# Kernel tuning notes

Hardware: AMD Instinct MI355X
Metric: run time of the kernel (lower is better)

Reference implementation:

```python
import jax, jax.numpy as jnp
import numpy as np

# Dims: B docs, L tokens, D hidden, H heads, NE padded entities (min_height),
# M mentions per entity, P entity pairs per doc, BLK bilinear block, NL labels.
B, L, D, H, NE, M, P = 4, 1024, 768, 12, 42, 4, 512
BLK, NL = 64, 97
OFFSET = 1  # self.offset = 1 (CLS token shift)


def setup_inputs() -> dict:
    key = jax.random.key(0)
    ks = jax.random.split(key, 10)
    sequence_output = jax.random.normal(ks[0], (B, L, D), jnp.float32)
    att = jax.random.uniform(ks[1], (B, H, L, L), jnp.float32)
    attention = att / att.sum(-1, keepdims=True)  # row-stochastic like softmax attn
    mention_pos = jax.random.randint(ks[2], (B, NE, M), 0, 1000, dtype=jnp.int32)
    hts = jax.random.randint(ks[3], (B, P, 2), 0, NE, dtype=jnp.int32)
    W_head = jax.random.normal(ks[4], (2 * D, D), jnp.float32) * 0.02
    b_head = jnp.zeros((D,), jnp.float32)
    W_tail = jax.random.normal(ks[5], (2 * D, D), jnp.float32) * 0.02
    b_tail = jnp.zeros((D,), jnp.float32)
    W_bi = jax.random.normal(ks[6], (D * BLK, NL), jnp.float32) * 0.02
    b_bi = jnp.zeros((NL,), jnp.float32)
    return dict(sequence_output=sequence_output, attention=attention,
                mention_pos=mention_pos, hts=hts,
                W_head=W_head, b_head=b_head, W_tail=W_tail, b_tail=b_tail,
                W_bi=W_bi, b_bi=b_bi)


def reference(sequence_output, attention, mention_pos, hts,
              W_head, b_head, W_tail, b_tail, W_bi, b_bi):
    pos = mention_pos + OFFSET                               # [B,NE,M]
    # --- get_hrt: entity embeds = logsumexp over mention start tokens ---
    e_emb = jax.vmap(lambda s, p: s[p])(sequence_output, pos)    # [B,NE,M,D]
    entity_embs = jax.nn.logsumexp(e_emb, axis=2)                # [B,NE,D]
    # entity attention = mean over mentions of attn rows           [B,NE,H,L]
    e_att = jax.vmap(lambda a, p: a[:, p])(attention, pos)       # [B,H,NE,M,L]
    entity_atts = e_att.mean(3).transpose(0, 2, 1, 3)            # [B,NE,H,L]
    # --- get_channel_map: ht_att = (h_att * t_att).mean(heads), normalized ---
    ht_att = jnp.einsum('bihl,bjhl->bijl', entity_atts, entity_atts) / H  # [B,NE,NE,L]
    ht_att = ht_att / (ht_att.sum(-1, keepdims=True) + 1e-5)
    rs_map = jnp.einsum('bijl,bld->bijd', ht_att, sequence_output)        # [B,NE,NE,D]
    # --- gather head/tail entity embeds and pooled context per pair ---
    h_idx, t_idx = hts[..., 0], hts[..., 1]                      # [B,P]
    hs = jnp.take_along_axis(entity_embs, h_idx[..., None], axis=1)  # [B,P,D]
    ts = jnp.take_along_axis(entity_embs, t_idx[..., None], axis=1)  # [B,P,D]
    rs = jax.vmap(lambda m, h, t: m[h, t])(rs_map, h_idx, t_idx)     # [B,P,D]
    # --- extractors + grouped bilinear classifier ---
    zs = jnp.tanh(jnp.concatenate([hs, rs], -1) @ W_head + b_head)   # [B,P,D]
    zo = jnp.tanh(jnp.concatenate([ts, rs], -1) @ W_tail + b_tail)   # [B,P,D]
    b1 = zs.reshape(B, P, D // BLK, BLK)
    b2 = zo.reshape(B, P, D // BLK, BLK)
    bl = (b1[..., :, None] * b2[..., None, :]).reshape(B, P, D * BLK)
    logits = bl @ W_bi + b_bi                                        # [B,P,NL]
    return logits
```

## Files before the change

### kernel.cpp

```cpp
#include <hip/hip_runtime.h>

constexpr int Bc = 4, Lc = 1024, Dc = 768, Hc = 12, NEc = 42, Mc = 4, Pc = 512, NLc = 97;
constexpr int BE   = Bc * NEc;
constexpr int BEp  = 176;
constexpr int ROWS = Bc * Pc;
constexpr int N2   = 2 * Dc;

typedef __attribute__((ext_vector_type(8))) short short8;
typedef _Float16 half8 __attribute__((ext_vector_type(8)));
typedef __attribute__((ext_vector_type(4))) float f32x4;

__device__ __forceinline__ f32x4 mfma_bf(short8 a, short8 b, f32x4 c) {
    return __builtin_amdgcn_mfma_f32_16x16x32_bf16(a, b, c, 0, 0, 0);
}
__device__ __forceinline__ f32x4 mfma_h(half8 a, half8 b, f32x4 c) {
    return __builtin_amdgcn_mfma_f32_16x16x32_f16(a, b, c, 0, 0, 0);
}
__device__ __forceinline__ unsigned short f2bf(float x) {
    unsigned int u = __float_as_uint(x);
    return (unsigned short)((u + 0x7fffu + ((u >> 16) & 1u)) >> 16);
}
__device__ __forceinline__ float bf2f(unsigned short h) {
    return __uint_as_float(((unsigned int)h) << 16);
}
__device__ __forceinline__ short8 ld8(const unsigned short* p) {
    return *(const short8*)(const void*)p;
}
__device__ __forceinline__ half8 ldh8(const _Float16* p) {
    return *(const half8*)(const void*)p;
}


constexpr int PB_EMBS  = 0;
constexpr int PB_EATT  = PB_EMBS + BEp;
constexpr int PB_TRSEQ = PB_EATT + BE * Hc;
constexpr int PB_TRW   = PB_TRSEQ + 768;
constexpr int PB_TRWBI = PB_TRW + 576;
constexpr int PB_ZERO  = PB_TRWBI + 768;
constexpr int PB_TOTAL = PB_ZERO + 97;

__global__ __launch_bounds__(256) void k_prep(const float* __restrict__ seq,
                                              const float* __restrict__ att,
                                              const int* __restrict__ mpos,
                                              const float* __restrict__ Wh,
                                              const float* __restrict__ Wt,
                                              const float* __restrict__ wbi,
                                              unsigned short* __restrict__ ep,
                                              unsigned short* __restrict__ eatt,
                                              unsigned short* __restrict__ sp,
                                              unsigned short* __restrict__ wp1,
                                              unsigned short* __restrict__ wp2,
                                              _Float16* __restrict__ wbp,
                                              float* __restrict__ out_zero) {
    __shared__ float smem[64 * 97];
    int blk = blockIdx.x;
    int t = threadIdx.x;

    if (blk < PB_EATT) {
        int be = blk - PB_EMBS, mt = be >> 4, lm = be & 15;
        float vals[3] = {0.f, 0.f, 0.f};
        if (be < BE) {
            int b = be / NEc;
            const int* pp = mpos + be * Mc;
            int p0 = pp[0] + 1, p1 = pp[1] + 1, p2 = pp[2] + 1, p3 = pp[3] + 1;
            const float* s = seq + (size_t)b * Lc * Dc;
            #pragma unroll
            for (int i = 0; i < 3; ++i) {
                int d = t + i * 256;
                float x0 = s[(size_t)p0 * Dc + d], x1 = s[(size_t)p1 * Dc + d];
                float x2 = s[(size_t)p2 * Dc + d], x3 = s[(size_t)p3 * Dc + d];
                float mx = fmaxf(fmaxf(x0, x1), fmaxf(x2, x3));
                vals[i] = mx + logf(expf(x0 - mx) + expf(x1 - mx) + expf(x2 - mx) + expf(x3 - mx));
            }
        }
        #pragma unroll
        for (int i = 0; i < 3; ++i) {
            int d = t + i * 256;
            int idx = ((mt * 24 + (d >> 5)) << 9) + (((d >> 3) & 3) << 7) + (lm << 3) + (d & 7);
            ep[idx] = f2bf(vals[i]);
        }
    } else if (blk < PB_TRSEQ) {
        int idx = blk - PB_EATT;
        int be = idx / Hc, h = idx - be * Hc, b = be / NEc;
        const int* pp = mpos + be * Mc;
        const float* a = att + ((size_t)(b * Hc + h)) * Lc * Lc;
        const float4* r0 = (const float4*)(a + (size_t)(pp[0] + 1) * Lc);
        const float4* r1 = (const float4*)(a + (size_t)(pp[1] + 1) * Lc);
        const float4* r2 = (const float4*)(a + (size_t)(pp[2] + 1) * Lc);
        const float4* r3 = (const float4*)(a + (size_t)(pp[3] + 1) * Lc);
        unsigned short* o = eatt + ((size_t)be * Hc + h) * Lc;
        float4 v0 = r0[t], v1 = r1[t], v2 = r2[t], v3 = r3[t];
        o[t * 4 + 0] = f2bf(0.25f * (v0.x + v1.x + v2.x + v3.x));
        o[t * 4 + 1] = f2bf(0.25f * (v0.y + v1.y + v2.y + v3.y));
        o[t * 4 + 2] = f2bf(0.25f * (v0.z + v1.z + v2.z + v3.z));
        o[t * 4 + 3] = f2bf(0.25f * (v0.w + v1.w + v2.w + v3.w));
    } else if (blk < PB_TRW) {
        int idx = blk - PB_TRSEQ;
        int xb = idx & 15, yb = (idx >> 4) % 12, b = idx / 192;
        int l0 = xb * 64, d0 = yb * 64;
        const float* s = seq + (size_t)b * Lc * Dc;
        #pragma unroll
        for (int i = 0; i < 16; ++i) {
            int ii = t + i * 256, r = ii >> 6, c = ii & 63;
            smem[r * 65 + c] = s[(size_t)(l0 + r) * Dc + d0 + c];
        }
        __syncthreads();
        unsigned short* outb = sp + (size_t)b * 48 * 32 * 512;
        int flat = t * 2, lane = flat >> 3, j = flat & 7;
        #pragma unroll
        for (int nt_i = 0; nt_i < 4; ++nt_i)
            #pragma unroll
            for (int kb_i = 0; kb_i < 2; ++kb_i) {
                int kl = kb_i * 32 + (lane >> 4) * 8 + j;
                int c  = nt_i * 16 + (lane & 15);
                unsigned int v = (unsigned)f2bf(smem[kl * 65 + c]) |
                                 ((unsigned)f2bf(smem[(kl + 1) * 65 + c]) << 16);
                *(unsigned int*)&outb[(((d0 / 16 + nt_i) * 32 + (l0 / 32 + kb_i)) << 9) + flat] = v;
            }
    } else if (blk < PB_TRWBI) {
        int idx = blk - PB_TRW;
        int xb = idx % 24, yb = (idx / 24) % 12, which = idx / 288;
        int k0 = xb * 64, n0 = yb * 64;
        const float* W = which ? Wt : Wh;
        #pragma unroll
        for (int i = 0; i < 16; ++i) {
            int ii = t + i * 256, r = ii >> 6, c = ii & 63;
            smem[r * 65 + c] = W[(size_t)(k0 + r) * Dc + n0 + c];
        }
        __syncthreads();
        unsigned short* dst = (k0 < Dc) ? wp1 : wp2;
        int kb0 = ((k0 < Dc) ? k0 : (k0 - Dc)) / 32;
        int nt0 = which * 48 + n0 / 16;
        int flat = t * 2, lane = flat >> 3, j = flat & 7;
        #pragma unroll
        for (int nt_i = 0; nt_i < 4; ++nt_i)
            #pragma unroll
            for (int kb_i = 0; kb_i < 2; ++kb_i) {
                int kl = kb_i * 32 + (lane >> 4) * 8 + j;
                int c  = nt_i * 16 + (lane & 15);
                unsigned int v = (unsigned)f2bf(smem[kl * 65 + c]) |
                                 ((unsigned)f2bf(smem[(kl + 1) * 65 + c]) << 16);
                *(unsigned int*)&dst[(((nt0 + nt_i) * 24 + kb0 + kb_i) << 9) + flat] = v;
            }
    } else if (blk < PB_ZERO) {
        int idx = blk - PB_TRWBI;
        int x = idx & 63, g = idx >> 6;
        const float* src = wbi + (size_t)(g * 4096 + x * 64) * NLc;
        for (int i = t; i < 64 * NLc; i += 256) smem[i] = src[i];
        __syncthreads();
        int flat = t * 2, lane = flat >> 3, j = flat & 7;
        int lm = lane & 15, qj = (lane >> 4) * 8 + j;
        #pragma unroll
        for (int nt = 0; nt < 7; ++nt)
            #pragma unroll
            for (int half = 0; half < 2; ++half) {
                int y = half * 32 + qj;
                int n = nt * 16 + lm;
                _Float16 v0 = (n < NLc) ? (_Float16)smem[y * NLc + n] : (_Float16)0.f;
                _Float16 v1 = (n < NLc) ? (_Float16)smem[(y + 1) * NLc + n] : (_Float16)0.f;
                size_t base = ((((size_t)(nt * 12 + g) * 64 + x) * 2 + half) << 9);
                _Float16* d = wbp + base + flat;
                d[0] = v0; d[1] = v1;
            }
    } else {
        int idx = blk - PB_ZERO;
        float4* o = (float4*)(out_zero + (size_t)idx * 2048);
        float4 z = {0.f, 0.f, 0.f, 0.f};
        o[t] = z;
        o[t + 256] = z;
    }
}

__global__ __launch_bounds__(256) void k_pairw(const unsigned short* __restrict__ eatt,
                                               const int* __restrict__ hts,
                                               unsigned short* __restrict__ pwp) {
    int bp = blockIdx.x, b = bp / Pc;
    int hi = hts[bp * 2], ti = hts[bp * 2 + 1];
    const unsigned short* ai = eatt + ((size_t)(b * NEc + hi)) * Hc * Lc;
    const unsigned short* aj = eatt + ((size_t)(b * NEc + ti)) * Hc * Lc;
    int l0 = threadIdx.x * 4;
    float acc[4] = {0.f, 0.f, 0.f, 0.f};
    #pragma unroll
    for (int h = 0; h < Hc; ++h) {
        uint2 ua = *(const uint2*)(ai + h * Lc + l0);
        uint2 ub = *(const uint2*)(aj + h * Lc + l0);
        acc[0] += bf2f(ua.x & 0xffff) * bf2f(ub.x & 0xffff);
        acc[1] += bf2f(ua.x >> 16)    * bf2f(ub.x >> 16);
        acc[2] += bf2f(ua.y & 0xffff) * bf2f(ub.y & 0xffff);
        acc[3] += bf2f(ua.y >> 16)    * bf2f(ub.y >> 16);
    }
    float lsum = acc[0] + acc[1] + acc[2] + acc[3];
    #pragma unroll
    for (int off = 32; off > 0; off >>= 1) lsum += __shfl_down(lsum, off, 64);
    __shared__ float red[4];
    __shared__ float sinv;
    int lane = threadIdx.x & 63, wv = threadIdx.x >> 6;
    if (lane == 0) red[wv] = lsum;
    __syncthreads();
    if (threadIdx.x == 0) sinv = 1.f / (red[0] + red[1] + red[2] + red[3] + 1.2e-4f);
    __syncthreads();
    float s = sinv;
    unsigned short w0 = f2bf(acc[0] * s), w1 = f2bf(acc[1] * s);
    unsigned short w2 = f2bf(acc[2] * s), w3 = f2bf(acc[3] * s);
    int mt = bp >> 4, lm = bp & 15, kb = l0 >> 5, quad = (l0 >> 3) & 3, j0 = l0 & 7;
    unsigned short* dst = pwp + ((mt * 32 + kb) << 9) + (quad << 7) + (lm << 3) + j0;
    *(uint2*)dst = make_uint2((unsigned)w0 | ((unsigned)w1 << 16),
                              (unsigned)w2 | ((unsigned)w3 << 16));
}

__global__ __launch_bounds__(256) void k_rsE(const unsigned short* __restrict__ pwp,
                                             const unsigned short* __restrict__ sp,
                                             const unsigned short* __restrict__ ep,
                                             const unsigned short* __restrict__ wp1,
                                             unsigned short* __restrict__ rsp,
                                             unsigned short* __restrict__ E) {
    int tid = threadIdx.x, wave = tid >> 6, lane = tid & 63;
    int quad = lane >> 4, lm = lane & 15;
    int blk = blockIdx.x;
    if (blk < 384) {
        int mb = blk & 7, ntq = (blk >> 3) % 12, b = blk / 96;
        int nt = ntq * 4 + wave;
        int mt0 = b * 32 + mb * 4;
        const unsigned short* bbase = sp + (((size_t)b * 48 + nt) * 32 << 9) + lane * 8;
        const unsigned short* abase = pwp + ((size_t)mt0 * 32 << 9) + lane * 8;
        f32x4 acc[4] = {};
        for (int kb = 0; kb < 32; ++kb) {
            short8 bf = ld8(bbase + kb * 512);
            #pragma unroll
            for (int mf = 0; mf < 4; ++mf)
                acc[mf] = mfma_bf(ld8(abase + (mf * 32 + kb) * 512), bf, acc[mf]);
        }
        int n = nt * 16 + lm, kbo = n >> 5, lq = ((n >> 3) & 3) << 4, jo = n & 7;
        #pragma unroll
        for (int mf = 0; mf < 4; ++mf) {
            unsigned short* db = rsp + (((mt0 + mf) * 24 + kbo) << 9) + jo;
            #pragma unroll
            for (int r = 0; r < 4; ++r)
                db[(lq + quad * 4 + r) << 3] = f2bf(acc[mf][r]);
        }
    } else {
        int idx = blk - 384;
        int mt = idx % 11, ntq = idx / 11;
        int nt = ntq * 4 + wave;
        const unsigned short* ab = ep + (mt * 24 << 9) + lane * 8;
        const unsigned short* bb = wp1 + (nt * 24 << 9) + lane * 8;
        f32x4 acc = {};
        for (int kb = 0; kb < 24; ++kb)
            acc = mfma_bf(ld8(ab + kb * 512), ld8(bb + kb * 512), acc);
        #pragma unroll
        for (int r = 0; r < 4; ++r)
            E[(size_t)(mt * 16 + quad * 4 + r) * N2 + nt * 16 + lm] = f2bf(acc[r]);
    }
}

__global__ __launch_bounds__(256) void k_Rz(const unsigned short* __restrict__ rsp,
                                            const unsigned short* __restrict__ wp2,
                                            const unsigned short* __restrict__ E,
                                            const int* __restrict__ hts,
                                            const float* __restrict__ bh,
                                            const float* __restrict__ bt,
                                            _Float16* __restrict__ zs,
                                            _Float16* __restrict__ zop) {
    int tid = threadIdx.x, wave = tid >> 6, lane = tid & 63;
    int quad = lane >> 4, lm = lane & 15;
    int mt0 = blockIdx.x * 4, nt = blockIdx.y * 4 + wave;
    const unsigned short* bb = wp2 + (nt * 24 << 9) + lane * 8;
    const unsigned short* ab = rsp + ((size_t)mt0 * 24 << 9) + lane * 8;
    f32x4 acc[4] = {};
    for (int kb = 0; kb < 24; ++kb) {
        short8 bf = ld8(bb + kb * 512);
        #pragma unroll
        for (int mf = 0; mf < 4; ++mf)
            acc[mf] = mfma_bf(ld8(ab + (mf * 24 + kb) * 512), bf, acc[mf]);
    }
    int np = nt * 16 + lm;
    bool is_zs = (np < Dc);
    int n = is_zs ? np : np - Dc;
    float bias = is_zs ? bh[n] : bt[n];
    #pragma unroll
    for (int mf = 0; mf < 4; ++mf) {
        int rowbase = (mt0 + mf) * 16 + quad * 4;
        #pragma unroll
        for (int r = 0; r < 4; ++r) {
            int row = rowbase + r;
            int b = row >> 9;
            int hh = hts[row * 2], tt = hts[row * 2 + 1];
            int ent = is_zs ? hh : tt;
            float ev = bf2f(E[(size_t)(b * NEc + ent) * N2 + np]);
            float v = tanhf(ev + acc[mf][r] + bias);
            if (is_zs) {
                zs[(size_t)row * Dc + n] = (_Float16)v;
            } else {
                int idx = (((row >> 4) * 24 + (n >> 5)) << 9) +
                          (((((n >> 3) & 3) << 4) + (row & 15)) << 3) + (n & 7);
                zop[idx] = (_Float16)v;
            }
        }
    }
}

__global__ __launch_bounds__(256) void k_bilin(const _Float16* __restrict__ zs,
                                               const _Float16* __restrict__ zop,
                                               const _Float16* __restrict__ wbp,
                                               const float* __restrict__ bbi,
                                               float* __restrict__ out) {
    __shared__ _Float16 zlds[256 * 72];
    int tid = threadIdx.x, wave = tid >> 6, lane = tid & 63;
    int quad = lane >> 4, lm = lane & 15;
    int pb = blockIdx.x, nt = blockIdx.y, g = blockIdx.z;
    {
        const half8* src = (const half8*)(zs + ((size_t)(pb * 256 + tid)) * Dc + g * 64);
        half8* dst = (half8*)&zlds[tid * 72];
        #pragma unroll
        for (int c = 0; c < 8; ++c) dst[c] = src[c];
    }
    __syncthreads();
    int mt0 = pb * 16 + wave * 4;
    half8 zofr[4][2];
    #pragma unroll
    for (int mf = 0; mf < 4; ++mf)
        #pragma unroll
        for (int hf = 0; hf < 2; ++hf)
            zofr[mf][hf] = ldh8(zop + (((mt0 + mf) * 24 + g * 2 + hf) << 9) + lane * 8);
    const _Float16* wbase = wbp + ((size_t)(nt * 12 + g) << 16) + lane * 8;
    const _Float16* zrow = &zlds[(wave * 64 + lm) * 72];
    f32x4 acc[4] = {};
    for (int x = 0; x < 64; ++x) {
        half8 b0 = ldh8(wbase + x * 1024);
        half8 b1 = ldh8(wbase + x * 1024 + 512);
        #pragma unroll
        for (int mf = 0; mf < 4; ++mf) {
            _Float16 s = zrow[mf * 16 * 72 + x];
            half8 bc = {s, s, s, s, s, s, s, s};
            acc[mf] = mfma_h(bc * zofr[mf][0], b0, acc[mf]);
            acc[mf] = mfma_h(bc * zofr[mf][1], b1, acc[mf]);
        }
    }
    int n = nt * 16 + lm;
    if (n < NLc) {
        #pragma unroll
        for (int mf = 0; mf < 4; ++mf)
            #pragma unroll
            for (int r = 0; r < 4; ++r) {
                int row = (mt0 + mf) * 16 + quad * 4 + r;
                float v = acc[mf][r];
                if (g == 0) v += bbi[n];
                atomicAdd(out + (size_t)row * NLc + n, v);
            }
    }
}

extern "C" void kernel_launch(void* const* d_in, const int* in_sizes, int n_in,
                              void* d_out, int out_size, void* d_ws, size_t ws_size,
                              hipStream_t stream) {
    const float* seq  = (const float*)d_in[0];
    const float* att  = (const float*)d_in[1];
    const int*   mpos = (const int*)d_in[2];
    const int*   hts  = (const int*)d_in[3];
    const float* Wh   = (const float*)d_in[4];
    const float* bh   = (const float*)d_in[5];
    const float* Wt   = (const float*)d_in[6];
    const float* bt   = (const float*)d_in[7];
    const float* Wbi  = (const float*)d_in[8];
    const float* bbi  = (const float*)d_in[9];
    float* out = (float*)d_out;

    char* w = (char*)d_ws;
    unsigned short* embs_p = (unsigned short*)(w);
    unsigned short* eatt_b = (unsigned short*)(w + 270336);
    unsigned short* pw_p   = (unsigned short*)(w + 4399104);
    unsigned short* seq_p  = (unsigned short*)(w + 8593408);
    _Float16*       wbi_p  = (_Float16*)(w + 14884864);
    unsigned short* wp1    = (unsigned short*)(w + 25894912);
    unsigned short* wp2    = (unsigned short*)(w + 28254208);
    unsigned short* E      = (unsigned short*)(w + 30613504);
    unsigned short* rs_p   = (unsigned short*)(w + 31154176);
    _Float16*       zs     = (_Float16*)(w + 34299904);
    _Float16*       zo_p   = (_Float16*)(w + 37445632);

    k_prep <<<PB_TOTAL, 256, 0, stream>>>(seq, att, mpos, Wh, Wt, Wbi,
                                          embs_p, eatt_b, seq_p, wp1, wp2, wbi_p, out);
    k_pairw<<<ROWS, 256, 0, stream>>>(eatt_b, hts, pw_p);
    k_rsE  <<<648, 256, 0, stream>>>(pw_p, seq_p, embs_p, wp1, rs_p, E);
    k_Rz   <<<dim3(32, 24), 256, 0, stream>>>(rs_p, wp2, E, hts, bh, bt, zs, zo_p);
    k_bilin<<<dim3(8, 7, 12), 256, 0, stream>>>(zs, zo_p, wbi_p, bbi, out);
}
```

Baseline: 374.5 us.

## Restructure bilinear kernel to reuse A fragments across all label tiles

Rewrites the bilinear classifier kernel so that each block covers all 7 label tiles, reusing the broadcast-scaled z fragments across them instead of recomputing them per label tile. Work is now split over 2 row-halves and 2 halves of the x reduction rather than over label tiles, giving 384 blocks in place of 672. The A-operand multiplies are amortized over more MFMAs, at the cost of more accumulator registers (14 f32x4) and twice the atomic adds to the output from the split reduction.

```diff
diff --git a/kernel.cpp b/kernel.cpp
--- a/kernel.cpp
+++ b/kernel.cpp
@@ -307,7 +307,8 @@
     __shared__ _Float16 zlds[256 * 72];
     int tid = threadIdx.x, wave = tid >> 6, lane = tid & 63;
     int quad = lane >> 4, lm = lane & 15;
-    int pb = blockIdx.x, nt = blockIdx.y, g = blockIdx.z;
+    int pb = blockIdx.x, g = blockIdx.y, z = blockIdx.z;
+    int mfh = z & 1, xh = z >> 1;
     {
         const half8* src = (const half8*)(zs + ((size_t)(pb * 256 + tid)) * Dc + g * 64);
         half8* dst = (half8*)&zlds[tid * 72];
@@ -315,38 +316,52 @@
         for (int c = 0; c < 8; ++c) dst[c] = src[c];
     }
     __syncthreads();
-    int mt0 = pb * 16 + wave * 4;
-    half8 zofr[4][2];
+    int mt0 = pb * 16 + wave * 4 + mfh * 2;
+    half8 zofr0[2], zofr1[2];
     #pragma unroll
-    for (int mf = 0; mf < 4; ++mf)
-        #pragma unroll
-        for (int hf = 0; hf < 2; ++hf)
-            zofr[mf][hf] = ldh8(zop + (((mt0 + mf) * 24 + g * 2 + hf) << 9) + lane * 8);
-    const _Float16* wbase = wbp + ((size_t)(nt * 12 + g) << 16) + lane * 8;
-    const _Float16* zrow = &zlds[(wave * 64 + lm) * 72];
-    f32x4 acc[4] = {};
-    for (int x = 0; x < 64; ++x) {
-        half8 b0 = ldh8(wbase + x * 1024);
-        half8 b1 = ldh8(wbase + x * 1024 + 512);
-        #pragma unroll
-        for (int mf = 0; mf < 4; ++mf) {
-            _Float16 s = zrow[mf * 16 * 72 + x];
-            half8 bc = {s, s, s, s, s, s, s, s};
-            acc[mf] = mfma_h(bc * zofr[mf][0], b0, acc[mf]);
-            acc[mf] = mfma_h(bc * zofr[mf][1], b1, acc[mf]);
-        }
-    }
-    int n = nt * 16 + lm;
-    if (n < NLc) {
-        #pragma unroll
-        for (int mf = 0; mf < 4; ++mf)
+    for (int hf = 0; hf < 2; ++hf) {
+        zofr0[hf] = ldh8(zop + (((mt0 + 0) * 24 + g * 2 + hf) << 9) + lane * 8);
+        zofr1[hf] = ldh8(zop + (((mt0 + 1) * 24 + g * 2 + hf) << 9) + lane * 8);
+    }
+    const _Float16* wg = wbp + ((size_t)g << 16) + lane * 8;
+    const _Float16* zrow = &zlds[(size_t)(wave * 64 + mfh * 32 + lm) * 72];
+    f32x4 acc0[7] = {};
+    f32x4 acc1[7] = {};
+    for (int xi = 0; xi < 32; ++xi) {
+        int x = xh * 32 + xi;
+        _Float16 s0 = zrow[x];
+        _Float16 s1 = zrow[16 * 72 + x];
+        half8 bc0 = {s0, s0, s0, s0, s0, s0, s0, s0};
+        half8 bc1 = {s1, s1, s1, s1, s1, s1, s1, s1};
+        half8 a00 = bc0 * zofr0[0];
+        half8 a01 = bc0 * zofr0[1];
+        half8 a10 = bc1 * zofr1[0];
+        half8 a11 = bc1 * zofr1[1];
+        const _Float16* wx = wg + (size_t)x * 1024;
+        #pragma unroll
+        for (int nt = 0; nt < 7; ++nt) {
+            const _Float16* p = wx + ((size_t)(nt * 12) << 16);
+            half8 b0 = ldh8(p);
+            half8 b1 = ldh8(p + 512);
+            acc0[nt] = mfma_h(a00, b0, acc0[nt]);
+            acc0[nt] = mfma_h(a01, b1, acc0[nt]);
+            acc1[nt] = mfma_h(a10, b0, acc1[nt]);
+            acc1[nt] = mfma_h(a11, b1, acc1[nt]);
+        }
+    }
+    #pragma unroll
+    for (int nt = 0; nt < 7; ++nt) {
+        int n = nt * 16 + lm;
+        if (n < NLc) {
+            float bias = (g == 0 && xh == 0) ? bbi[n] : 0.f;
             #pragma unroll
             for (int r = 0; r < 4; ++r) {
-                int row = (mt0 + mf) * 16 + quad * 4 + r;
-                float v = acc[mf][r];
-                if (g == 0) v += bbi[n];
-                atomicAdd(out + (size_t)row * NLc + n, v);
-            }
+                int row0 = (mt0 + 0) * 16 + quad * 4 + r;
+                int row1 = (mt0 + 1) * 16 + quad * 4 + r;
+                atomicAdd(out + (size_t)row0 * NLc + n, acc0[nt][r] + bias);
+                atomicAdd(out + (size_t)row1 * NLc + n, acc1[nt][r] + bias);
+            }
+        }
     }
 }
 
@@ -383,5 +398,5 @@
     k_pairw<<<ROWS, 256, 0, stream>>>(eatt_b, hts, pw_p);
     k_rsE  <<<648, 256, 0, stream>>>(pw_p, seq_p, embs_p, wp1, rs_p, E);
     k_Rz   <<<dim3(32, 24), 256, 0, stream>>>(rs_p, wp2, E, hts, bh, bt, zs, zo_p);
-    k_bilin<<<dim3(8, 7, 12), 256, 0, stream>>>(zs, zo_p, wbi_p, bbi, out);
-}
+    k_bilin<<<dim3(8, 12, 4), 256, 0, stream>>>(zs, zo_p, wbi_p, bbi, out);
+}
```

New measurement: 425.7 us. +13.7%, slower.
